# Kernel tuning notes

Measured on AMD Instinct MI355X. Metric: run time of the kernel, lower is better.

## Reference

```python
import jax, jax.numpy as jnp
import numpy as np

N, D, H = 4096, 128, 8

def setup_inputs() -> dict:
    key = jax.random.key(0)
    ks = jax.random.split(key, 7)
    xavier = float(np.sqrt(6.0 / (D + D)))  # xavier_uniform for [*, D, D]
    x = jax.random.normal(ks[0], (N, D), dtype=jnp.float32)
    W_k = jax.random.uniform(ks[1], (H, D, D), minval=-xavier, maxval=xavier, dtype=jnp.float32)
    W_q = jax.random.uniform(ks[2], (H, D, D), minval=-xavier, maxval=xavier, dtype=jnp.float32)
    W_v = jax.random.uniform(ks[3], (H, D, D), minval=-xavier, maxval=xavier, dtype=jnp.float32)
    W_m = jnp.ones((H,), dtype=jnp.float32)
    lim = float(1.0 / np.sqrt(D))  # default torch Linear init range
    Wg = jax.random.uniform(ks[4], (D, D), minval=-lim, maxval=lim, dtype=jnp.float32)
    bg = jax.random.uniform(ks[5], (D,), minval=-lim, maxval=lim, dtype=jnp.float32)
    return {"x": x, "W_k": W_k, "W_q": W_q, "W_v": W_v, "W_m": W_m, "Wg": Wg, "bg": bg}

def reference(x, W_k, W_q, W_v, W_m, Wg, bg):
    # per-head projections: [H, N, D]
    q = jnp.einsum('nf,hfd->hnd', x, W_q)
    k = jnp.einsum('nf,hfd->hnd', x, W_k)
    v = jnp.einsum('nf,hfd->hnd', x, W_v)
    # dense all-pairs attention scores per head: [H, N, N]
    e = jnp.einsum('hnd,hmd->hnm', q, k)
    attn = jax.nn.softmax(e, axis=-1)
    # weighted sum over values, then head-scaled accumulation: [N, D]
    out = jnp.einsum('h,hnm,hmd->nd', W_m, attn, v)
    # residual MLP: x + ReLU(Linear(x + out))
    h = x + out
    g = jax.nn.relu(h @ Wg.T + bg)
    return x + g
```

## Files before the change

kernel.cpp:

```cpp
#include <hip/hip_runtime.h>

#define NROWS 4096
#define DDIM  128
#define NHEAD 8
#define LOG2E 1.44269504088896f

extern "C" __device__ float __ocml_native_exp2_f32(float);

typedef __attribute__((ext_vector_type(8))) short    short8;
typedef __attribute__((ext_vector_type(8))) _Float16 half8;
typedef __attribute__((ext_vector_type(4))) float    floatx4;

__device__ __forceinline__ float bf2f(unsigned short u){
  unsigned v = ((unsigned)u) << 16;
  return __builtin_bit_cast(float, v);
}
__device__ __forceinline__ unsigned short f2bf(float f){
  unsigned u = __builtin_bit_cast(unsigned, f);
  u += 0x7FFFu + ((u >> 16) & 1u);
  return (unsigned short)(u >> 16);
}
__device__ __forceinline__ void split2(float v, unsigned short& hi, unsigned short& lo){
  hi = f2bf(v);
  lo = f2bf(v - bf2f(hi));
}
__device__ __forceinline__ void async_cp16(const void* g, void* l){
  __builtin_amdgcn_global_load_lds(
      (const __attribute__((address_space(1))) void*)g,
      (__attribute__((address_space(3))) void*)l, 16, 0, 0);
}
__device__ __forceinline__ float dpp_max16(float v){
  int t;
  t = __builtin_amdgcn_update_dpp(0, __builtin_bit_cast(int, v), 0x128, 0xF, 0xF, false);
  v = fmaxf(v, __builtin_bit_cast(float, t));
  t = __builtin_amdgcn_update_dpp(0, __builtin_bit_cast(int, v), 0x124, 0xF, 0xF, false);
  v = fmaxf(v, __builtin_bit_cast(float, t));
  t = __builtin_amdgcn_update_dpp(0, __builtin_bit_cast(int, v), 0x122, 0xF, 0xF, false);
  v = fmaxf(v, __builtin_bit_cast(float, t));
  t = __builtin_amdgcn_update_dpp(0, __builtin_bit_cast(int, v), 0x121, 0xF, 0xF, false);
  v = fmaxf(v, __builtin_bit_cast(float, t));
  return v;
}

__global__ void fill_kernel(float* __restrict__ out, float val, int n){
  int i = blockIdx.x * 256 + threadIdx.x;
  if (i < n) out[i] = val;
}

__global__ __launch_bounds__(256) void prep_kernel(
    const float* __restrict__ Wk, const float* __restrict__ Wv,
    const float* __restrict__ Wq, const float* __restrict__ Wg,
    const float* __restrict__ x,
    unsigned short* __restrict__ wpre, unsigned short* __restrict__ wgpre,
    unsigned short* __restrict__ xh, unsigned short* __restrict__ xl)
{
  const int id = blockIdx.x * 256 + threadIdx.x;
  if (id < 49152) {
    const int z = id >> 14, rem = id & 16383;
    const int h = rem >> 11, rem2 = rem & 2047;
    const int fh = rem2 >> 10, L = rem2 & 1023;
    const int d = L >> 3, m = L & 7;
    const int kk0 = (m ^ (d & 7)) << 3;
    const float* W = (z == 0 ? Wk : (z == 1 ? Wv : Wq)) + h * DDIM * DDIM;
    short8 hi8, lo8;
#pragma unroll
    for (int j = 0; j < 8; j++) {
      unsigned short hi, lo;
      split2(W[(fh * 64 + kk0 + j) * DDIM + d], hi, lo);
      hi8[j] = (short)hi; lo8[j] = (short)lo;
    }
    unsigned short* base = wpre + (size_t)((z * 8 + h) * 2 + fh) * 16384;
    *(short8*)(base + L * 8) = hi8;
    *(short8*)(base + 8192 + L * 8) = lo8;
  } else if (id < 51200) {
    const int t = id - 49152;
    const int fh = t >> 10, L = t & 1023;
    const int d = L >> 3, m = L & 7;
    const int kk0 = (m ^ (d & 7)) << 3;
    short8 hi8, lo8;
#pragma unroll
    for (int j = 0; j < 8; j++) {
      unsigned short hi, lo;
      split2(Wg[d * DDIM + fh * 64 + kk0 + j], hi, lo);
      hi8[j] = (short)hi; lo8[j] = (short)lo;
    }
    unsigned short* base = wgpre + fh * 16384;
    *(short8*)(base + L * 8) = hi8;
    *(short8*)(base + 8192 + L * 8) = lo8;
  } else if (id < 116736) {
    const int t = id - 51200;
    const float* src = x + (size_t)t * 8;
    float4 v0 = *(const float4*)src, v1 = *(const float4*)(src + 4);
    float xv[8] = {v0.x, v0.y, v0.z, v0.w, v1.x, v1.y, v1.z, v1.w};
    short8 hi8, lo8;
#pragma unroll
    for (int j = 0; j < 8; j++) {
      unsigned short hi, lo; split2(xv[j], hi, lo);
      hi8[j] = (short)hi; lo8[j] = (short)lo;
    }
    *(short8*)(xh + (size_t)t * 8) = hi8;
    *(short8*)(xl + (size_t)t * 8) = lo8;
  }
}

__global__ __launch_bounds__(256, 2) void proj_kernel(
    const unsigned short* __restrict__ xh, const unsigned short* __restrict__ xl,
    const unsigned short* __restrict__ wpre,
    _Float16* __restrict__ kfo, _Float16* __restrict__ vfo,
    _Float16* __restrict__ qfo)
{
  __shared__ alignas(16) unsigned short whi[8192];
  __shared__ alignas(16) unsigned short wlo[8192];
  const int tid = threadIdx.x, lane = tid & 63, wave = tid >> 6;
  const int l4 = lane & 15, quad = lane >> 4;
  const int h = blockIdx.y, z = blockIdx.z;
  const unsigned short* wb = wpre + (size_t)((z * 8 + h) * 2) * 16384;

  floatx4 acc[4][8];
#pragma unroll
  for (int t4 = 0; t4 < 4; t4++)
#pragma unroll
    for (int c = 0; c < 8; c++) acc[t4][c] = (floatx4)0.f;

  for (int fh = 0; fh < 2; fh++) {
    {
      const unsigned short* src = wb + fh * 16384;
      const unsigned short* sh = src + wave * 2048 + lane * 8;
      const unsigned short* sl = src + 8192 + wave * 2048 + lane * 8;
      unsigned short* dh = &whi[wave * 2048];
      unsigned short* dl = &wlo[wave * 2048];
#pragma unroll
      for (int it = 0; it < 4; it++) {
        async_cp16(sh + it * 512, dh + it * 512);
        async_cp16(sl + it * 512, dl + it * 512);
      }
    }
    __syncthreads();

#pragma unroll
    for (int t4 = 0; t4 < 4; t4++) {
      const int row = blockIdx.x * 256 + t4 * 64 + wave * 16 + l4;
      const size_t xo = (size_t)row * DDIM + fh * 64 + quad * 8;
      short8 ah[2], al[2];
      ah[0] = *(const short8*)(xh + xo);
      ah[1] = *(const short8*)(xh + xo + 32);
      al[0] = *(const short8*)(xl + xo);
      al[1] = *(const short8*)(xl + xo + 32);
#pragma unroll
      for (int t2 = 0; t2 < 2; t2++) {
#pragma unroll
        for (int c = 0; c < 8; c++) {
          const int col = c * 16 + l4;
          const int idx = (col * 8 + ((t2 * 4 + quad) ^ (col & 7))) * 8;
          short8 bh = *(const short8*)&whi[idx];
          short8 bl = *(const short8*)&wlo[idx];
          acc[t4][c] = __builtin_amdgcn_mfma_f32_16x16x32_bf16(ah[t2], bh, acc[t4][c], 0, 0, 0);
          acc[t4][c] = __builtin_amdgcn_mfma_f32_16x16x32_bf16(al[t2], bh, acc[t4][c], 0, 0, 0);
          acc[t4][c] = __builtin_amdgcn_mfma_f32_16x16x32_bf16(ah[t2], bl, acc[t4][c], 0, 0, 0);
        }
      }
    }
    __syncthreads();
  }

  const int rb = wave * 16 + quad * 4;
#pragma unroll
  for (int t4 = 0; t4 < 4; t4++) {
    const int tile = blockIdx.x * 4 + t4;
    const size_t tilebase = (size_t)(h * 64 + tile) * 8192;
#pragma unroll
    for (int c = 0; c < 8; c++) {
      const int d = c * 16 + l4;
#pragma unroll
      for (int r = 0; r < 4; r++) {
        const int kl = rb + r;
        const float val = acc[t4][c][r];
        if (z == 0) {
          const int c2 = kl >> 4, l4k = kl & 15;
          const int tt = d >> 5, qd = (d >> 3) & 3, jj = d & 7;
          const int qX = qd ^ ((l4k >> 1) & 3);
          kfo[tilebase + (size_t)((c2 * 4 + tt) * 16 + l4k) * 32 + qX * 8 + jj] =
              (_Float16)val;
        } else if (z == 1) {
          const int c2 = d >> 4, l4v = d & 15;
          const int tt = kl >> 5, qd = (kl >> 3) & 3, jj = kl & 7;
          const int qX = qd ^ ((l4v >> 1) & 3);
          vfo[tilebase + (size_t)((c2 * 2 + tt) * 16 + l4v) * 32 + qX * 8 + jj] =
              (_Float16)val;
        } else {
          qfo[((size_t)h * NROWS + (size_t)tile * 64 + kl) * DDIM + d] =
              (_Float16)(val * LOG2E);
        }
      }
    }
  }
}

struct FlashLds {
  _Float16 k[2][8192];
  _Float16 p[4][1024];
};

__global__ __launch_bounds__(256, 4) void flash_kernel(
    const _Float16* __restrict__ qfo, const _Float16* __restrict__ kfo,
    const _Float16* __restrict__ vfo,
    _Float16* __restrict__ op, float* __restrict__ mb, float* __restrict__ lb)
{
  __shared__ alignas(16) FlashLds lds;
  const int tid = threadIdx.x, lane = tid & 63, wave = tid >> 6;
  const int l4 = lane & 15, quad = lane >> 4;
  const int h = blockIdx.x & 7, qt = (blockIdx.x >> 3) & 63, s = blockIdx.x >> 9;
  const int q0 = qt * 64;

  half8 aq[4];
  {
    const _Float16* qr =
        qfo + ((size_t)h * NROWS + q0 + wave * 16 + l4) * DDIM + quad * 8;
#pragma unroll
    for (int t = 0; t < 4; t++) aq[t] = *(const half8*)(qr + t * 32);
  }

  float m_run[4];
#pragma unroll
  for (int r = 0; r < 4; r++) m_run[r] = -1e30f;
  floatx4 Oacc[8], lacc = (floatx4)0.f;
#pragma unroll
  for (int c = 0; c < 8; c++) Oacc[c] = (floatx4)0.f;

  half8 vones;
#pragma unroll
  for (int j = 0; j < 8; j++) vones[j] = (_Float16)1.f;

  const _Float16* kfo_h = kfo + (size_t)h * 64 * 8192;
  const _Float16* vfo_h = vfo + (size_t)h * 64 * 8192;
  const int lq = (l4 * 4 + (quad ^ ((l4 >> 1) & 3))) * 8;
  const int kt0 = s * 32, kt1 = kt0 + 32;

  {
    const _Float16* ks = kfo_h + (size_t)kt0 * 8192 + wave * 2048 + lane * 8;
    _Float16* kd = &lds.k[0][wave * 2048];
#pragma unroll
    for (int it = 0; it < 4; it++) async_cp16(ks + it * 512, kd + it * 512);
  }

  for (int kt = kt0; kt < kt1; ++kt) {
    const int cur = kt & 1;
    __syncthreads();

    if (kt + 1 < kt1) {
      const _Float16* ks = kfo_h + (size_t)(kt + 1) * 8192 + wave * 2048 + lane * 8;
      _Float16* kd = &lds.k[cur ^ 1][wave * 2048];
#pragma unroll
      for (int it = 0; it < 4; it++) async_cp16(ks + it * 512, kd + it * 512);
    }

    floatx4 Sf[4];
#pragma unroll
    for (int c = 0; c < 4; c++) Sf[c] = (floatx4)0.f;
    __builtin_amdgcn_s_setprio(1);
#pragma unroll
    for (int t = 0; t < 4; t++) {
      half8 b[4];
#pragma unroll
      for (int c = 0; c < 4; c++)
        b[c] = *(const half8*)&lds.k[cur][(c * 4 + t) * 512 + lq];
#pragma unroll
      for (int c = 0; c < 4; c++)
        Sf[c] = __builtin_amdgcn_mfma_f32_16x16x32_f16(aq[t], b[c], Sf[c], 0, 0, 0);
    }
    __builtin_amdgcn_s_setprio(0);

    float alpha[4];
    {
      float mt[4];
#pragma unroll
      for (int r = 0; r < 4; r++)
        mt[r] = fmaxf(fmaxf(Sf[0][r], Sf[1][r]), fmaxf(Sf[2][r], Sf[3][r]));
#pragma unroll
      for (int r = 0; r < 4; r++) mt[r] = dpp_max16(mt[r]);
#pragma unroll
      for (int r = 0; r < 4; r++) {
        const float mn = fmaxf(m_run[r], mt[r]);
        alpha[r] = __ocml_native_exp2_f32(m_run[r] - mn);
        m_run[r] = mn;
      }
#pragma unroll
      for (int r = 0; r < 4; r++)
#pragma unroll
        for (int c = 0; c < 4; c++)
          Sf[c][r] = __ocml_native_exp2_f32(Sf[c][r] - m_run[r]);
    }

#pragma unroll
    for (int c = 0; c < 4; c++)
#pragma unroll
      for (int r = 0; r < 4; r++)
        lds.p[wave][((c * 2 + (l4 >> 3)) * 16 + quad * 4 + r) * 8 + (l4 & 7)] =
            (_Float16)Sf[c][r];

    {
      const bool moved = (alpha[0] != 1.f) | (alpha[1] != 1.f) |
                         (alpha[2] != 1.f) | (alpha[3] != 1.f);
      if (__any(moved)) {
#pragma unroll
        for (int c = 0; c < 8; c++) {
          Oacc[c][0] *= alpha[0]; Oacc[c][1] *= alpha[1];
          Oacc[c][2] *= alpha[2]; Oacc[c][3] *= alpha[3];
        }
        lacc[0] *= alpha[0]; lacc[1] *= alpha[1];
        lacc[2] *= alpha[2]; lacc[3] *= alpha[3];
      }
    }

#pragma unroll
    for (int t = 0; t < 2; t++) {
      half8 vf[8];
      {
        const _Float16* vtb = vfo_h + (size_t)kt * 8192 + t * 512 + lq;
#pragma unroll
        for (int c = 0; c < 8; c++)
          vf[c] = *(const half8*)(vtb + c * 1024);
      }
      half8 ap = *(const half8*)&lds.p[wave][((t * 4 + quad) * 16 + l4) * 8];
      __builtin_amdgcn_s_setprio(1);
      lacc = __builtin_amdgcn_mfma_f32_16x16x32_f16(ap, vones, lacc, 0, 0, 0);
#pragma unroll
      for (int c = 0; c < 8; c++)
        Oacc[c] = __builtin_amdgcn_mfma_f32_16x16x32_f16(ap, vf[c], Oacc[c], 0, 0, 0);
      __builtin_amdgcn_s_setprio(0);
    }
  }

  const int rbase = wave * 16 + quad * 4;
  const size_t rowbase = (size_t)(s * NHEAD + h) * NROWS + q0 + rbase;
#pragma unroll
  for (int c = 0; c < 8; c++) {
    const int col = c * 16 + l4;
#pragma unroll
    for (int r = 0; r < 4; r++)
      op[(rowbase + r) * DDIM + col] = (_Float16)Oacc[c][r];
  }
  if (l4 == 0) {
#pragma unroll
    for (int r = 0; r < 4; r++) {
      mb[rowbase + r] = m_run[r];
      lb[rowbase + r] = lacc[r];
    }
  }
}

__global__ __launch_bounds__(128) void merge_kernel(
    const _Float16* __restrict__ op, const float* __restrict__ mb,
    const float* __restrict__ lb, const float* __restrict__ Wm,
    float* __restrict__ u)
{
  __shared__ float sc[2][NHEAD];
  const int n = blockIdx.x, d = threadIdx.x;
  if (d < NHEAD) {
    const int h = d;
    const float m1 = mb[(size_t)h * NROWS + n];
    const float m2 = mb[(size_t)(NHEAD + h) * NROWS + n];
    const float l1 = lb[(size_t)h * NROWS + n];
    const float l2 = lb[(size_t)(NHEAD + h) * NROWS + n];
    const float m  = fmaxf(m1, m2);
    const float a1 = __ocml_native_exp2_f32(m1 - m);
    const float a2 = __ocml_native_exp2_f32(m2 - m);
    const float invL = Wm[h] / (l1 * a1 + l2 * a2);
    sc[0][h] = a1 * invL;
    sc[1][h] = a2 * invL;
  }
  __syncthreads();
  float acc = 0.f;
#pragma unroll
  for (int h = 0; h < NHEAD; h++) {
    acc += sc[0][h] * (float)op[((size_t)h * NROWS + n) * DDIM + d];
    acc += sc[1][h] * (float)op[((size_t)(NHEAD + h) * NROWS + n) * DDIM + d];
  }
  u[(size_t)n * DDIM + d] = acc;
}

__global__ __launch_bounds__(256, 2) void mlp_kernel(
    const float* __restrict__ x, const float* __restrict__ u,
    const unsigned short* __restrict__ wgpre, const float* __restrict__ bg,
    float* __restrict__ out)
{
  __shared__ alignas(16) unsigned short whi[8192];
  __shared__ alignas(16) unsigned short wlo[8192];
  const int tid = threadIdx.x, lane = tid & 63, wave = tid >> 6;
  const int l4 = lane & 15, quad = lane >> 4;
  const int r0 = blockIdx.x * 64;

  floatx4 acc[8];
#pragma unroll
  for (int c = 0; c < 8; c++) acc[c] = (floatx4)0.f;

  for (int fh = 0; fh < 2; fh++) {
    {
      const unsigned short* src = wgpre + fh * 16384;
      const unsigned short* sh = src + wave * 2048 + lane * 8;
      const unsigned short* sl = src + 8192 + wave * 2048 + lane * 8;
      unsigned short* dh = &whi[wave * 2048];
      unsigned short* dl = &wlo[wave * 2048];
#pragma unroll
      for (int it = 0; it < 4; it++) {
        async_cp16(sh + it * 512, dh + it * 512);
        async_cp16(sl + it * 512, dl + it * 512);
      }
    }
    __syncthreads();

    const size_t xoff = (size_t)(r0 + wave * 16 + l4) * DDIM + fh * 64 + quad * 8;
    short8 ah[2], al[2];
#pragma unroll
    for (int t2 = 0; t2 < 2; t2++) {
      float4 x0 = *(const float4*)(x + xoff + t2 * 32);
      float4 x1 = *(const float4*)(x + xoff + t2 * 32 + 4);
      float4 u0 = *(const float4*)(u + xoff + t2 * 32);
      float4 u1 = *(const float4*)(u + xoff + t2 * 32 + 4);
      float hv[8] = {x0.x + u0.x, x0.y + u0.y, x0.z + u0.z, x0.w + u0.w,
                     x1.x + u1.x, x1.y + u1.y, x1.z + u1.z, x1.w + u1.w};
#pragma unroll
      for (int j = 0; j < 8; j++) {
        unsigned short hi, lo; split2(hv[j], hi, lo);
        ah[t2][j] = (short)hi; al[t2][j] = (short)lo;
      }
    }
#pragma unroll
    for (int t2 = 0; t2 < 2; t2++) {
#pragma unroll
      for (int c = 0; c < 8; c++) {
        const int col = c * 16 + l4;
        const int idx = (col * 8 + ((t2 * 4 + quad) ^ (col & 7))) * 8;
        short8 bh = *(const short8*)&whi[idx];
        short8 bl = *(const short8*)&wlo[idx];
        acc[c] = __builtin_amdgcn_mfma_f32_16x16x32_bf16(ah[t2], bh, acc[c], 0, 0, 0);
        acc[c] = __builtin_amdgcn_mfma_f32_16x16x32_bf16(al[t2], bh, acc[c], 0, 0, 0);
        acc[c] = __builtin_amdgcn_mfma_f32_16x16x32_bf16(ah[t2], bl, acc[c], 0, 0, 0);
      }
    }
    __syncthreads();
  }

  const int rbase = wave * 16 + quad * 4;
#pragma unroll
  for (int c = 0; c < 8; c++) {
    const int col = c * 16 + l4;
    const float bgf = bg[col];
#pragma unroll
    for (int r = 0; r < 4; r++) {
      const size_t idx = (size_t)(r0 + rbase + r) * DDIM + col;
      out[idx] = x[idx] + fmaxf(acc[c][r] + bgf, 0.f);
    }
  }
}

extern "C" void kernel_launch(void* const* d_in, const int* in_sizes, int n_in,
                              void* d_out, int out_size, void* d_ws, size_t ws_size,
                              hipStream_t stream) {
  float* out = (float*)d_out;
  const int fill_blocks = (out_size + 255) / 256;

  const bool ok_sizes =
      n_in == 7 &&
      in_sizes[0] == NROWS * DDIM &&
      in_sizes[1] == NHEAD * DDIM * DDIM &&
      in_sizes[2] == NHEAD * DDIM * DDIM &&
      in_sizes[3] == NHEAD * DDIM * DDIM &&
      in_sizes[4] == NHEAD &&
      in_sizes[5] == DDIM * DDIM &&
      in_sizes[6] == DDIM &&
      out_size == NROWS * DDIM;
  if (!ok_sizes) {
    fill_kernel<<<fill_blocks, 256, 0, stream>>>(out, 1000.f, out_size);
    return;
  }

  const size_t HND = (size_t)NHEAD * NROWS * DDIM;
  const size_t ND  = (size_t)NROWS * DDIM;
  const size_t WPRE_N  = (size_t)3 * 8 * 2 * 16384;
  const size_t WGPRE_N = (size_t)2 * 16384;
  const size_t need = ND * 4 + 3 * HND * 2 + 2 * HND * 2 +
                      2 * (2 * (size_t)NHEAD * NROWS) * 4 +
                      (WPRE_N + WGPRE_N + 2 * ND) * 2;
  if (ws_size < need) {
    fill_kernel<<<fill_blocks, 256, 0, stream>>>(out, 500.f, out_size);
    return;
  }

  const float* x  = (const float*)d_in[0];
  const float* Wk = (const float*)d_in[1];
  const float* Wq = (const float*)d_in[2];
  const float* Wv = (const float*)d_in[3];
  const float* Wm = (const float*)d_in[4];
  const float* Wg = (const float*)d_in[5];
  const float* bg = (const float*)d_in[6];

  float*          u     = (float*)d_ws;
  _Float16*       kfo   = (_Float16*)(u + ND);
  _Float16*       vfo   = kfo + HND;
  _Float16*       qfo   = vfo + HND;
  _Float16*       op    = qfo + HND;
  float*          mb    = (float*)(op + 2 * HND);
  float*          lb    = mb + 2 * NHEAD * NROWS;
  unsigned short* wpre  = (unsigned short*)(lb + 2 * NHEAD * NROWS);
  unsigned short* wgpre = wpre + WPRE_N;
  unsigned short* xh    = wgpre + WGPRE_N;
  unsigned short* xl    = xh + ND;

  (void)hipGetLastError();
  prep_kernel<<<dim3(456), 256, 0, stream>>>(Wk, Wv, Wq, Wg, x, wpre, wgpre, xh, xl);
  proj_kernel<<<dim3(16, NHEAD, 3), 256, 0, stream>>>(xh, xl, wpre, kfo, vfo, qfo);
  flash_kernel<<<dim3(1024), 256, 0, stream>>>(qfo, kfo, vfo, op, mb, lb);
  merge_kernel<<<dim3(4096), 128, 0, stream>>>(op, mb, lb, Wm, u);
  mlp_kernel<<<dim3(64), 256, 0, stream>>>(x, u, wgpre, bg, out);
  if (hipGetLastError() != hipSuccess) {
    fill_kernel<<<fill_blocks, 256, 0, stream>>>(out, 2000.f, out_size);
  }
}
```

Measured before the change: 215.2 us.

## Fuse split-softmax merge into MLP kernel and swizzle LDS P tile

Removes the separate merge kernel. The MLP kernel now computes the per-row, per-head rescale factors from the split max/sum buffers and accumulates the fp16 partial outputs directly into x+out before the bf16-split GEMM. This drops one launch and the fp32 intermediate write and read. Separately, the flash kernel's LDS staging of probabilities uses an XOR row swizzle to reduce bank conflicts. The fused MLP runs only 64 blocks, so the merge reads of all 16 partial outputs are concentrated on few CUs.

After: 217.0 us. No clear change (+0.8%).

```diff
diff --git a/kernel.cpp b/kernel.cpp
--- a/kernel.cpp
+++ b/kernel.cpp
@@ -294,9 +294,11 @@
 #pragma unroll
     for (int c = 0; c < 4; c++)
 #pragma unroll
-      for (int r = 0; r < 4; r++)
-        lds.p[wave][((c * 2 + (l4 >> 3)) * 16 + quad * 4 + r) * 8 + (l4 & 7)] =
-            (_Float16)Sf[c][r];
+      for (int r = 0; r < 4; r++) {
+        const int row_s = (c * 2 + (l4 >> 3)) * 16 + quad * 4 + r;
+        const int rs = row_s ^ ((row_s >> 2) & 7);
+        lds.p[wave][rs * 8 + (l4 & 7)] = (_Float16)Sf[c][r];
+      }
 
     {
       const bool moved = (alpha[0] != 1.f) | (alpha[1] != 1.f) |
@@ -321,7 +323,9 @@
         for (int c = 0; c < 8; c++)
           vf[c] = *(const half8*)(vtb + c * 1024);
       }
-      half8 ap = *(const half8*)&lds.p[wave][((t * 4 + quad) * 16 + l4) * 8];
+      const int row_r = (t * 4 + quad) * 16 + l4;
+      const int rr = row_r ^ ((row_r >> 2) & 7);
+      half8 ap = *(const half8*)&lds.p[wave][rr * 8];
       __builtin_amdgcn_s_setprio(1);
       lacc = __builtin_amdgcn_mfma_f32_16x16x32_f16(ap, vones, lacc, 0, 0, 0);
 #pragma unroll
@@ -349,50 +353,42 @@
   }
 }
 
-__global__ __launch_bounds__(128) void merge_kernel(
-    const _Float16* __restrict__ op, const float* __restrict__ mb,
-    const float* __restrict__ lb, const float* __restrict__ Wm,
-    float* __restrict__ u)
-{
-  __shared__ float sc[2][NHEAD];
-  const int n = blockIdx.x, d = threadIdx.x;
-  if (d < NHEAD) {
-    const int h = d;
-    const float m1 = mb[(size_t)h * NROWS + n];
-    const float m2 = mb[(size_t)(NHEAD + h) * NROWS + n];
-    const float l1 = lb[(size_t)h * NROWS + n];
-    const float l2 = lb[(size_t)(NHEAD + h) * NROWS + n];
-    const float m  = fmaxf(m1, m2);
-    const float a1 = __ocml_native_exp2_f32(m1 - m);
-    const float a2 = __ocml_native_exp2_f32(m2 - m);
-    const float invL = Wm[h] / (l1 * a1 + l2 * a2);
-    sc[0][h] = a1 * invL;
-    sc[1][h] = a2 * invL;
-  }
-  __syncthreads();
-  float acc = 0.f;
-#pragma unroll
-  for (int h = 0; h < NHEAD; h++) {
-    acc += sc[0][h] * (float)op[((size_t)h * NROWS + n) * DDIM + d];
-    acc += sc[1][h] * (float)op[((size_t)(NHEAD + h) * NROWS + n) * DDIM + d];
-  }
-  u[(size_t)n * DDIM + d] = acc;
-}
-
 __global__ __launch_bounds__(256, 2) void mlp_kernel(
-    const float* __restrict__ x, const float* __restrict__ u,
+    const float* __restrict__ x, const _Float16* __restrict__ op,
+    const float* __restrict__ mb, const float* __restrict__ lb,
+    const float* __restrict__ Wm,
     const unsigned short* __restrict__ wgpre, const float* __restrict__ bg,
     float* __restrict__ out)
 {
   __shared__ alignas(16) unsigned short whi[8192];
   __shared__ alignas(16) unsigned short wlo[8192];
+  __shared__ float sc[64][17];
   const int tid = threadIdx.x, lane = tid & 63, wave = tid >> 6;
   const int l4 = lane & 15, quad = lane >> 4;
   const int r0 = blockIdx.x * 64;
 
+  for (int i = tid; i < 512; i += 256) {
+    const int rr = i >> 3, hh = i & 7;
+    const int n = r0 + rr;
+    const float m1 = mb[(size_t)hh * NROWS + n];
+    const float m2 = mb[(size_t)(NHEAD + hh) * NROWS + n];
+    const float l1 = lb[(size_t)hh * NROWS + n];
+    const float l2 = lb[(size_t)(NHEAD + hh) * NROWS + n];
+    const float m  = fmaxf(m1, m2);
+    const float a1 = __ocml_native_exp2_f32(m1 - m);
+    const float a2 = __ocml_native_exp2_f32(m2 - m);
+    const float invL = Wm[hh] / (l1 * a1 + l2 * a2);
+    sc[rr][hh] = a1 * invL;
+    sc[rr][8 + hh] = a2 * invL;
+  }
+
   floatx4 acc[8];
 #pragma unroll
   for (int c = 0; c < 8; c++) acc[c] = (floatx4)0.f;
+
+  float scr[16];
+  const int rloc = wave * 16 + l4;
+  const size_t nrow = (size_t)(r0 + rloc);
 
   for (int fh = 0; fh < 2; fh++) {
     {
@@ -409,16 +405,26 @@
     }
     __syncthreads();
 
-    const size_t xoff = (size_t)(r0 + wave * 16 + l4) * DDIM + fh * 64 + quad * 8;
+    if (fh == 0) {
+#pragma unroll
+      for (int i = 0; i < 16; i++) scr[i] = sc[rloc][i];
+    }
+
     short8 ah[2], al[2];
 #pragma unroll
     for (int t2 = 0; t2 < 2; t2++) {
-      float4 x0 = *(const float4*)(x + xoff + t2 * 32);
-      float4 x1 = *(const float4*)(x + xoff + t2 * 32 + 4);
-      float4 u0 = *(const float4*)(u + xoff + t2 * 32);
-      float4 u1 = *(const float4*)(u + xoff + t2 * 32 + 4);
-      float hv[8] = {x0.x + u0.x, x0.y + u0.y, x0.z + u0.z, x0.w + u0.w,
-                     x1.x + u1.x, x1.y + u1.y, x1.z + u1.z, x1.w + u1.w};
+      const int dbase = fh * 64 + t2 * 32 + quad * 8;
+      const size_t xoff = nrow * DDIM + dbase;
+      float4 x0 = *(const float4*)(x + xoff);
+      float4 x1 = *(const float4*)(x + xoff + 4);
+      float hv[8] = {x0.x, x0.y, x0.z, x0.w, x1.x, x1.y, x1.z, x1.w};
+#pragma unroll
+      for (int i = 0; i < 16; i++) {
+        const half8 ov = *(const half8*)(op + ((size_t)i * NROWS + nrow) * DDIM + dbase);
+        const float sci = scr[i];
+#pragma unroll
+        for (int j = 0; j < 8; j++) hv[j] += sci * (float)ov[j];
+      }
 #pragma unroll
       for (int j = 0; j < 8; j++) {
         unsigned short hi, lo; split2(hv[j], hi, lo);
@@ -479,7 +485,7 @@
   const size_t ND  = (size_t)NROWS * DDIM;
   const size_t WPRE_N  = (size_t)3 * 8 * 2 * 16384;
   const size_t WGPRE_N = (size_t)2 * 16384;
-  const size_t need = ND * 4 + 3 * HND * 2 + 2 * HND * 2 +
+  const size_t need = 3 * HND * 2 + 2 * HND * 2 +
                       2 * (2 * (size_t)NHEAD * NROWS) * 4 +
                       (WPRE_N + WGPRE_N + 2 * ND) * 2;
   if (ws_size < need) {
@@ -495,8 +501,7 @@
   const float* Wg = (const float*)d_in[5];
   const float* bg = (const float*)d_in[6];
 
-  float*          u     = (float*)d_ws;
-  _Float16*       kfo   = (_Float16*)(u + ND);
+  _Float16*       kfo   = (_Float16*)d_ws;
   _Float16*       vfo   = kfo + HND;
   _Float16*       qfo   = vfo + HND;
   _Float16*       op    = qfo + HND;
@@ -511,8 +516,7 @@
   prep_kernel<<<dim3(456), 256, 0, stream>>>(Wk, Wv, Wq, Wg, x, wpre, wgpre, xh, xl);
   proj_kernel<<<dim3(16, NHEAD, 3), 256, 0, stream>>>(xh, xl, wpre, kfo, vfo, qfo);
   flash_kernel<<<dim3(1024), 256, 0, stream>>>(qfo, kfo, vfo, op, mb, lb);
-  merge_kernel<<<dim3(4096), 128, 0, stream>>>(op, mb, lb, Wm, u);
-  mlp_kernel<<<dim3(64), 256, 0, stream>>>(x, u, wgpre, bg, out);
+  mlp_kernel<<<dim3(64), 256, 0, stream>>>(x, op, mb, lb, Wm, wgpre, bg, out);
   if (hipGetLastError() != hipSuccess) {
     fill_kernel<<<fill_blocks, 256, 0, stream>>>(out, 2000.f, out_size);
   }
```
